# Kernel optimization log

Measured on AMD Instinct MI355X. Metric: run time of the kernel, lower is better.

The kernel has to match this reference:

```python
import jax, jax.numpy as jnp
import numpy as np

N, N_H = 256, 64          # detections per image, humans (permuted to top)
NUM_ITER = 2
E = 1024                   # node_encoding_size == box_feature_size
T_LIS, K_LIS, W_LIS = 8.3, 12.0, 10.0


def lis(x):
    # Low-grade Instance Suppression
    return T_LIS / (1.0 + jnp.exp(K_LIS - W_LIS * x))


def setup_inputs() -> dict:
    key = jax.random.key(0)
    ks = jax.random.split(key, 25)
    s = 0.02  # weight scale keeps sigmoid/relu in a sane range
    rn = lambda k, shape, sc=1.0: jax.random.normal(k, shape, jnp.float32) * sc
    inp = {}
    inp['box_features'] = rn(ks[0], (N, 12544))            # [N, 256*7*7]
    inp['node_spatial'] = rn(ks[1], (N, 1024))             # conv spatial-head output
    inp['scores'] = jax.random.uniform(ks[2], (N,), jnp.float32)
    labels = jax.random.randint(ks[3], (N,), 1, 80)
    inp['labels'] = labels.at[:N_H].set(0)                 # humans (idx 0) on top
    inp['class_mask'] = jax.random.bernoulli(ks[4], 0.2, (80, 117))
    inp['W_bh1'] = rn(ks[5], (12544, 1024), s); inp['b_bh1'] = jnp.zeros((1024,), jnp.float32)
    inp['W_bh2'] = rn(ks[6], (1024, 1024), s);  inp['b_bh2'] = jnp.zeros((1024,), jnp.float32)
    inp['W_sa']  = rn(ks[7], (1024, 1024), s)
    inp['W_a1']  = rn(ks[8], (4096, 2048), s); inp['b_a1'] = jnp.zeros((2048,), jnp.float32)
    inp['W_a2']  = rn(ks[9], (2048, 1024), s); inp['b_a2'] = jnp.zeros((1024,), jnp.float32)
    inp['W_a3']  = rn(ks[10], (1024, 1), s);   inp['b_a3'] = jnp.zeros((1,), jnp.float32)
    inp['W_hm']  = rn(ks[11], (1024, 1024), s); inp['b_hm'] = jnp.zeros((1024,), jnp.float32)
    inp['W_om']  = rn(ks[12], (1024, 1024), s); inp['b_om'] = jnp.zeros((1024,), jnp.float32)
    inp['W_hu']  = rn(ks[13], (2048, 1024), s)
    inp['W_ou']  = rn(ks[14], (2048, 1024), s)
    return inp


def _keep_indices():
    xv, yv = np.meshgrid(np.arange(N_H), np.arange(N), indexing='ij')
    m = (xv != yv).ravel()
    return jnp.asarray(xv.ravel()[m]), jnp.asarray(yv.ravel()[m])


def reference(box_features, node_spatial, scores, W_bh1, b_bh1, W_bh2, b_bh2,
              W_sa, W_a1, b_a1, W_a2, b_a2, W_a3, b_a3,
              W_hm, b_hm, W_om, b_om, W_hu, W_ou, labels, class_mask):
    # box_head: Flatten -> Linear -> ReLU -> Linear -> ReLU
    enc = jax.nn.relu(box_features @ W_bh1 + b_bh1)
    enc = jax.nn.relu(enc @ W_bh2 + b_bh2)                 # [N, E]
    h_enc = enc[:N_H]                                      # [N_H, E]
    h_sp = node_spatial[:N_H]                              # [N_H, 1024]
    # spatial_attention on pairwise spatial differences (fixed across iters)
    diff = node_spatial[None, :, :] - h_sp[:, None, :]     # [N_H, N, 1024]
    h_to_o = jnp.einsum('hnd,de->hne', diff, W_sa)         # Linear, no bias
    o_to_h = -h_to_o
    adj = jnp.ones((N_H, N), enc.dtype)
    for _ in range(NUM_ITER):
        # adjacency MLP + sigmoid over all n_h*n pairs
        hf = jnp.concatenate([h_enc, h_sp], axis=1)        # [N_H, 2048]
        of = jnp.concatenate([enc, node_spatial], axis=1)  # [N, 2048]
        pair_in = jnp.concatenate([
            jnp.broadcast_to(hf[:, None, :], (N_H, N, 2 * E)),
            jnp.broadcast_to(of[None, :, :], (N_H, N, 2 * E))], axis=-1)  # [N_H,N,4096]
        hdn = jax.nn.relu(pair_in @ W_a1 + b_a1)
        hdn = jax.nn.relu(hdn @ W_a2 + b_a2)
        adj = jax.nn.sigmoid((hdn @ W_a3 + b_a3)[..., 0])  # [N_H, N]
        # object -> human messages
        obj_msg = jax.nn.relu(enc @ W_om + b_om)           # [N, R]
        agg_o = (adj[..., None] * (obj_msg[None, :, :] * o_to_h)).sum(1)  # [N_H, R]
        h_enc = jnp.concatenate([h_enc, agg_o], axis=1) @ W_hu            # [N_H, E]
        # human -> object messages
        hum_msg = jax.nn.relu(h_enc @ W_hm + b_hm)         # [N_H, R]
        agg_h = (adj[..., None] * (hum_msg[:, None, :] * h_to_o)).sum(0)  # [N, R]
        enc = jnp.concatenate([enc, agg_h], axis=1) @ W_ou                # [N, E]
    x_keep, y_keep = _keep_indices()                       # [P], P = N_H*N - N_H
    pair_feats = jnp.concatenate([h_enc[x_keep], h_sp[x_keep],
                                  enc[y_keep], node_spatial[y_keep]], axis=1)  # [P, 4096]
    # prior scores: LIS(score_h)*LIS(score_o) scattered to valid target classes
    prod = lis(scores[x_keep]) * lis(scores[y_keep])       # [P]
    prior = prod[:, None] * class_mask[labels[y_keep]].astype(pair_feats.dtype)  # [P, 117]
    prior = adj[x_keep, y_keep][:, None] * prior
    return jnp.concatenate([pair_feats, prior], axis=1)    # [P, 4096+117]
```

## Files before the change

### kernel.cpp

```cpp
#include <hip/hip_runtime.h>

using bf16 = __bf16;
typedef __bf16 bf16x4 __attribute__((ext_vector_type(4)));
typedef __bf16 bf16x8 __attribute__((ext_vector_type(8)));
typedef float  f32x4  __attribute__((ext_vector_type(4)));

#define LDS_STRIDE 40
#define GST 40

__device__ __forceinline__ float ldf(const void* p, size_t i, int f32) {
    return f32 ? ((const float*)p)[i] : (float)((const bf16*)p)[i];
}
__device__ __forceinline__ bf16x8 ld8(const void* p, size_t i, int f32) {
    bf16x8 r;
    if (f32) {
        f32x4 a = *(const f32x4*)((const float*)p + i);
        f32x4 b = *(const f32x4*)((const float*)p + i + 4);
#pragma unroll
        for (int j = 0; j < 4; ++j) { r[j] = (bf16)a[j]; r[j + 4] = (bf16)b[j]; }
    } else {
        r = *(const bf16x8*)((const bf16*)p + i);
    }
    return r;
}
__device__ __forceinline__ void st1(void* p, size_t i, float v, int f32) {
    if (f32) ((float*)p)[i] = v;
    else     ((bf16*)p)[i] = (bf16)v;
}

__global__ void init_flag(int* __restrict__ dflag) { *dflag = 0; }

__global__ void detect_kernel(const unsigned short* __restrict__ p, int n,
                              int* __restrict__ dflag)
{
    const unsigned int* q = (const unsigned int*)p;
    const int nw = n >> 1;
    int hit = 0;
    for (int i = blockIdx.x * 256 + threadIdx.x; i < nw; i += gridDim.x * 256) {
        unsigned int w = q[i];
        if ((w & 0x7F80u) == 0x7F80u || (w & 0x7F800000u) == 0x7F800000u) hit = 1;
    }
    if (__any(hit) && (threadIdx.x & 63) == 0) atomicOr(dflag, 1);
}

__global__ void cvt_kernel(const void* __restrict__ src, bf16* __restrict__ dst,
                           int n, const int* __restrict__ dflag)
{
    const int f32 = *dflag;
    const int stride = gridDim.x * 256;
    if ((n & 7) == 0) {
        const int nv = n >> 3;
        for (int i = blockIdx.x * 256 + threadIdx.x; i < nv; i += stride) {
            bf16x8 v = ld8(src, (size_t)i * 8, f32);
            *(bf16x8*)(dst + (size_t)i * 8) = v;
        }
    } else {
        for (int i = blockIdx.x * 256 + threadIdx.x; i < n; i += stride)
            dst[i] = (bf16)ldf(src, i, f32);
    }
}

__global__ void transpose_any(const void* __restrict__ W, bf16* __restrict__ Wt,
                              int K, int N, const int* __restrict__ dflag)
{
    __shared__ bf16 tile[32][33];
    const int f32 = *dflag;
    const int n0 = blockIdx.x * 32, k0 = blockIdx.y * 32;
    const int tx = threadIdx.x, ty = threadIdx.y;
#pragma unroll
    for (int i = 0; i < 4; ++i)
        tile[ty + i * 8][tx] = (bf16)ldf(W, (size_t)(k0 + ty + i * 8) * N + n0 + tx, f32);
    __syncthreads();
#pragma unroll
    for (int i = 0; i < 4; ++i)
        Wt[(size_t)(n0 + ty + i * 8) * K + k0 + tx] = tile[tx][ty + i * 8];
}

__global__ __launch_bounds__(256)
void gemm_p(const bf16* __restrict__ A, int lda,
            const void* __restrict__ B, size_t boff, int ldb,
            float* __restrict__ part, int N, int Kc,
            const int* __restrict__ dflag)
{
    __shared__ bf16 As[64 * GST];
    __shared__ bf16 Bs[64 * GST];
    const int f32 = *dflag;
    const int t = threadIdx.x;
    const int l = t & 63;
    const int quad = l >> 4, lr = l & 15;
    const int w = t >> 6, wm = w >> 1, wn = w & 1;
    const int mBlock = blockIdx.y * 64, nBlock = blockIdx.x * 64;
    const int ar = t >> 2, ac = (t & 3) * 8;
    const int kr = t >> 3, nc = (t & 7) * 8;
    const int kBeg = blockIdx.z * Kc;
    const int nIter = Kc >> 5;

    f32x4 acc[2][2] = {};

    bf16x8 avr = *(const bf16x8*)(A + (size_t)(mBlock + ar) * lda + kBeg + ac);
    bf16x8 bvr = ld8(B, boff + (size_t)(kBeg + kr) * ldb + nBlock + nc, f32);

    for (int it = 0; it < nIter; ++it) {
        *(bf16x8*)&As[ar * GST + ac] = avr;
#pragma unroll
        for (int j = 0; j < 8; ++j) {
            int wr = nc + j;
            Bs[wr * GST + (kr ^ (((wr >> 3) & 3) << 3))] = bvr[j];
        }
        __syncthreads();
        if (it + 1 < nIter) {
            int k0 = kBeg + (it + 1) * 32;
            avr = *(const bf16x8*)(A + (size_t)(mBlock + ar) * lda + k0 + ac);
            bvr = ld8(B, boff + (size_t)(k0 + kr) * ldb + nBlock + nc, f32);
        }
        bf16x8 af[2], bfr[2];
#pragma unroll
        for (int mi = 0; mi < 2; ++mi)
            af[mi] = *(const bf16x8*)&As[(wm * 32 + mi * 16 + lr) * GST + quad * 8];
#pragma unroll
        for (int nj = 0; nj < 2; ++nj) {
            int row = wn * 32 + nj * 16 + lr;
            bfr[nj] = *(const bf16x8*)&Bs[row * GST + ((quad * 8) ^ (((row >> 3) & 3) << 3))];
        }
#pragma unroll
        for (int mi = 0; mi < 2; ++mi)
#pragma unroll
            for (int nj = 0; nj < 2; ++nj)
                acc[mi][nj] = __builtin_amdgcn_mfma_f32_16x16x32_bf16(
                    af[mi], bfr[nj], acc[mi][nj], 0, 0, 0);
        __syncthreads();
    }

    float* outp = part + (size_t)blockIdx.z * ((size_t)gridDim.y * 64 * N);
#pragma unroll
    for (int mi = 0; mi < 2; ++mi)
#pragma unroll
        for (int nj = 0; nj < 2; ++nj) {
            int col = nBlock + wn * 32 + nj * 16 + lr;
#pragma unroll
            for (int rr = 0; rr < 4; ++rr) {
                int row = mBlock + wm * 32 + mi * 16 + quad * 4 + rr;
                outp[(size_t)row * N + col] = acc[mi][nj][rr];
            }
        }
}

template<bool RELU, bool BIAS, bool F32OUT>
__global__ void reduce_k(const float* __restrict__ part, int S, int total,
                         const bf16* __restrict__ bias, void* __restrict__ out, int N)
{
    int base = (blockIdx.x * 256 + threadIdx.x) * 4;
    if (base >= total) return;
    f32x4 s = *(const f32x4*)(part + base);
    for (int z = 1; z < S; ++z) {
        f32x4 v = *(const f32x4*)(part + (size_t)z * total + base);
        s[0] += v[0]; s[1] += v[1]; s[2] += v[2]; s[3] += v[3];
    }
    int col = base % N;
#pragma unroll
    for (int j = 0; j < 4; ++j) {
        float v = s[j];
        if (BIAS) v += (float)bias[col + j];
        if (RELU) v = fmaxf(v, 0.f);
        if (F32OUT) ((float*)out)[base + j] = v;
        else        ((bf16*)out)[base + j] = (bf16)v;
    }
}

__global__ __launch_bounds__(256)
void pair_gemm(const float* __restrict__ Hpart, const float* __restrict__ Opart,
               const bf16* __restrict__ b_a1, const bf16* __restrict__ Wt_a2,
               const bf16* __restrict__ b_a2, const bf16* __restrict__ w_a3,
               float* __restrict__ slots)
{
    __shared__ bf16 As[128 * LDS_STRIDE];
    __shared__ bf16 Bs[128 * LDS_STRIDE];
    const int t = threadIdx.x;
    const int l = t & 63, w = t >> 6;
    const int quad = l >> 4, lr = l & 15;
    const int wm = w >> 1, wn = w & 1;
    const int nb = blockIdx.x, mb = blockIdx.y;
    const int p0 = mb * 128;
    const int h = p0 >> 8;
    const int nBase = p0 & 255;
    const int ar = t >> 1, ac0 = (t & 1) * 16;
    const float* Hrow = Hpart + h * 2048;
    const float* Orow = Opart + (size_t)(nBase + ar) * 2048;

    f32x4 acc[4][4] = {};

    for (int k0 = 0; k0 < 2048; k0 += 32) {
        __syncthreads();
        {
            const float* hp = Hrow + k0 + ac0;
            const float* op = Orow + k0 + ac0;
            f32x4 h0 = *(const f32x4*)(hp);
            f32x4 h1 = *(const f32x4*)(hp + 4);
            f32x4 h2 = *(const f32x4*)(hp + 8);
            f32x4 h3 = *(const f32x4*)(hp + 12);
            f32x4 o0 = *(const f32x4*)(op);
            f32x4 o1 = *(const f32x4*)(op + 4);
            f32x4 o2 = *(const f32x4*)(op + 8);
            f32x4 o3 = *(const f32x4*)(op + 12);
            bf16x8 r0, r1;
#pragma unroll
            for (int j = 0; j < 4; ++j) {
                r0[j]     = (bf16)fmaxf(h0[j] + o0[j] + (float)b_a1[k0 + ac0 + j],      0.f);
                r0[j + 4] = (bf16)fmaxf(h1[j] + o1[j] + (float)b_a1[k0 + ac0 + 4 + j],  0.f);
                r1[j]     = (bf16)fmaxf(h2[j] + o2[j] + (float)b_a1[k0 + ac0 + 8 + j],  0.f);
                r1[j + 4] = (bf16)fmaxf(h3[j] + o3[j] + (float)b_a1[k0 + ac0 + 12 + j], 0.f);
            }
            *(bf16x8*)&As[ar * LDS_STRIDE + ac0]     = r0;
            *(bf16x8*)&As[ar * LDS_STRIDE + ac0 + 8] = r1;
        }
#pragma unroll
        for (int i = 0; i < 2; ++i) {
            int idx = t + i * 256;
            int r = idx >> 2, c = (idx & 3) * 8;
            *(bf16x8*)&Bs[r * LDS_STRIDE + c] =
                *(const bf16x8*)(Wt_a2 + (size_t)(nb * 128 + r) * 2048 + k0 + c);
        }
        __syncthreads();

        bf16x8 af[4], bfr[4];
#pragma unroll
        for (int mi = 0; mi < 4; ++mi)
            af[mi] = *(const bf16x8*)&As[(wm * 64 + mi * 16 + lr) * LDS_STRIDE + quad * 8];
#pragma unroll
        for (int nj = 0; nj < 4; ++nj)
            bfr[nj] = *(const bf16x8*)&Bs[(wn * 64 + nj * 16 + lr) * LDS_STRIDE + quad * 8];
#pragma unroll
        for (int mi = 0; mi < 4; ++mi)
#pragma unroll
            for (int nj = 0; nj < 4; ++nj)
                acc[mi][nj] = __builtin_amdgcn_mfma_f32_16x16x32_bf16(
                    af[mi], bfr[nj], acc[mi][nj], 0, 0, 0);
    }

    float w3v[4], b2v[4];
#pragma unroll
    for (int nj = 0; nj < 4; ++nj) {
        int col = nb * 128 + wn * 64 + nj * 16 + lr;
        w3v[nj] = (float)w_a3[col];
        b2v[nj] = (float)b_a2[col];
    }
#pragma unroll
    for (int mi = 0; mi < 4; ++mi) {
        f32x4 rs = {0.f, 0.f, 0.f, 0.f};
#pragma unroll
        for (int nj = 0; nj < 4; ++nj)
#pragma unroll
            for (int rr = 0; rr < 4; ++rr)
                rs[rr] += fmaxf(acc[mi][nj][rr] + b2v[nj], 0.f) * w3v[nj];
#pragma unroll
        for (int off = 1; off < 16; off <<= 1) {
            rs[0] += __shfl_xor(rs[0], off);
            rs[1] += __shfl_xor(rs[1], off);
            rs[2] += __shfl_xor(rs[2], off);
            rs[3] += __shfl_xor(rs[3], off);
        }
        if (lr == 0) {
            int p = p0 + wm * 64 + mi * 16 + quad * 4;
            int slot = nb * 2 + wn;
            slots[(size_t)(p + 0) * 16 + slot] = rs[0];
            slots[(size_t)(p + 1) * 16 + slot] = rs[1];
            slots[(size_t)(p + 2) * 16 + slot] = rs[2];
            slots[(size_t)(p + 3) * 16 + slot] = rs[3];
        }
    }
}

__global__ void adj_finalize(const float* __restrict__ slots,
                             const bf16* __restrict__ b_a3, float* __restrict__ adj)
{
    int i = blockIdx.x * 256 + threadIdx.x;
    float s = (float)b_a3[0];
#pragma unroll
    for (int k = 0; k < 16; ++k) s += slots[(size_t)i * 16 + k];
    adj[i] = 1.f / (1.f + expf(-s));
}

__global__ void copy_rows(const bf16* __restrict__ src, int lds_,
                          bf16* __restrict__ dst, int ldd)
{
    int c = blockIdx.x * 256 + threadIdx.x;
    int r = blockIdx.y;
    dst[(size_t)r * ldd + c] = src[(size_t)r * lds_ + c];
}

__global__ void agg_o_kernel(const float* __restrict__ adj, const bf16* __restrict__ obj_msg,
                             const bf16* __restrict__ nsW, bf16* __restrict__ out)
{
    int e = blockIdx.x * 256 + threadIdx.x;
    int h = blockIdx.y;
    float nh = (float)nsW[h * 1024 + e];
    float s = 0.f;
    for (int n = 0; n < 256; ++n) {
        float a  = adj[h * 256 + n];
        float om = (float)obj_msg[n * 1024 + e];
        float nw = (float)nsW[n * 1024 + e];
        s += a * om * (nh - nw);
    }
    out[(size_t)h * 2048 + e] = (bf16)s;
}

__global__ void agg_h_kernel(const float* __restrict__ adj, const bf16* __restrict__ hum_msg,
                             const bf16* __restrict__ nsW, bf16* __restrict__ out)
{
    int e = blockIdx.x * 256 + threadIdx.x;
    int n = blockIdx.y;
    float nn = (float)nsW[n * 1024 + e];
    float s = 0.f;
    for (int h = 0; h < 64; ++h) {
        float a  = adj[h * 256 + n];
        float hm = (float)hum_msg[h * 1024 + e];
        float nw = (float)nsW[h * 1024 + e];
        s += a * hm * (nn - nw);
    }
    out[(size_t)n * 2048 + e] = (bf16)s;
}

__global__ void out_kernel(const bf16* __restrict__ h_enc, const bf16* __restrict__ enc,
                           const bf16* __restrict__ nsp_bf, const float* __restrict__ adj,
                           const bf16* __restrict__ scores_bf, const int* __restrict__ labels,
                           const int* __restrict__ cmask, void* __restrict__ out,
                           const int* __restrict__ dflag)
{
    const int f32 = *dflag;
    const int r = blockIdx.x;
    const int x = r / 255;
    const int tt = r % 255;
    const int y = tt + (tt >= x ? 1 : 0);
    const size_t rbase = (size_t)r * 4213;
    const bf16* seg[4] = { h_enc + x * 1024, nsp_bf + x * 1024, enc + y * 1024, nsp_bf + y * 1024 };
    const int t = threadIdx.x;
#pragma unroll
    for (int k = 0; k < 4; ++k) {
        int ci = t + k * 256;
        int sidx = ci >> 8;
        int off = (ci & 255) * 4;
        bf16x4 v = *(const bf16x4*)(seg[sidx] + off);
        size_t d = rbase + sidx * 1024 + off;
        st1(out, d + 0, (float)v[0], f32);
        st1(out, d + 1, (float)v[1], f32);
        st1(out, d + 2, (float)v[2], f32);
        st1(out, d + 3, (float)v[3], f32);
    }
    if (t < 117) {
        float sx = (float)scores_bf[x], sy = (float)scores_bf[y];
        float lx = 8.3f / (1.f + expf(12.f - 10.f * sx));
        float ly = 8.3f / (1.f + expf(12.f - 10.f * sy));
        float a = adj[x * 256 + y];
        float m = cmask[labels[y] * 117 + t] ? 1.f : 0.f;
        st1(out, rbase + 4096 + t, a * lx * ly * m, f32);
    }
}

extern "C" void kernel_launch(void* const* d_in, const int* in_sizes, int n_in,
                              void* d_out, int out_size, void* d_ws, size_t ws_size,
                              hipStream_t stream)
{
    (void)in_sizes; (void)n_in; (void)out_size; (void)ws_size;
    const void* box    = d_in[0];
    const void* nsp    = d_in[1];
    const void* scores = d_in[2];
    const int*  labels = (const int*)d_in[3];
    const int*  cmask  = (const int*)d_in[4];
    const void* W_bh1 = d_in[5],  *b_bh1 = d_in[6];
    const void* W_bh2 = d_in[7],  *b_bh2 = d_in[8];
    const void* W_sa  = d_in[9];
    const void* W_a1  = d_in[10], *b_a1  = d_in[11];
    const void* W_a2  = d_in[12], *b_a2  = d_in[13];
    const void* W_a3  = d_in[14], *b_a3  = d_in[15];
    const void* W_hm  = d_in[16], *b_hm  = d_in[17];
    const void* W_om  = d_in[18], *b_om  = d_in[19];
    const void* W_hu  = d_in[20];
    const void* W_ou  = d_in[21];

    char* ws = (char*)d_ws;
    size_t off = 0;
    auto alloc = [&](size_t bytes) -> void* {
        off = (off + 255) & ~(size_t)255;
        void* p = ws + off;
        off += bytes;
        return p;
    };
    int*  dflag   = (int*)alloc(4);
    bf16* box_bf  = (bf16*)alloc((size_t)256 * 12544 * 2);
    bf16* nsp_bf  = (bf16*)alloc((size_t)256 * 1024 * 2);
    bf16* Wt_a2   = (bf16*)alloc((size_t)1024 * 2048 * 2);
    bf16* smalls  = (bf16*)alloc((size_t)8464 * 2);
    bf16* sb_bh1 = smalls,        *sb_bh2 = smalls + 1024;
    bf16* sb_om  = smalls + 2048, *sb_hm  = smalls + 3072;
    bf16* sb_a1  = smalls + 4096, *sb_a2  = smalls + 6144;
    bf16* sw_a3  = smalls + 7168, *sb_a3  = smalls + 8192;
    bf16* sscore = smalls + 8208;
    bf16* t0      = (bf16*)alloc((size_t)256 * 1024 * 2);
    bf16* enc     = (bf16*)alloc((size_t)256 * 1024 * 2);
    bf16* nsW     = (bf16*)alloc((size_t)256 * 1024 * 2);
    bf16* h_enc   = (bf16*)alloc((size_t)64 * 1024 * 2);
    bf16* hf      = (bf16*)alloc((size_t)64 * 2048 * 2);
    bf16* of      = (bf16*)alloc((size_t)256 * 2048 * 2);
    float* Hpart  = (float*)alloc((size_t)64 * 2048 * 4);
    float* Opart  = (float*)alloc((size_t)256 * 2048 * 4);
    float* slots  = (float*)alloc((size_t)16384 * 16 * 4);
    float* adj    = (float*)alloc((size_t)16384 * 4);
    bf16* obj_msg = (bf16*)alloc((size_t)256 * 1024 * 2);
    bf16* hu_in   = (bf16*)alloc((size_t)64 * 2048 * 2);
    bf16* hum_msg = (bf16*)alloc((size_t)64 * 1024 * 2);
    bf16* ou_in   = (bf16*)alloc((size_t)256 * 2048 * 2);
    float* part   = (float*)alloc((size_t)2097152 * 4);

    init_flag<<<1, 1, 0, stream>>>(dflag);
    detect_kernel<<<256, 256, 0, stream>>>((const unsigned short*)box, 524288, dflag);

    auto cvt = [&](const void* s, bf16* d, int n) {
        int g = (n + 2047) / 2048; if (g < 1) g = 1; if (g > 4096) g = 4096;
        cvt_kernel<<<g, 256, 0, stream>>>(s, d, n, dflag);
    };
    cvt(box, box_bf, 256 * 12544);
    cvt(nsp, nsp_bf, 256 * 1024);
    cvt(b_bh1, sb_bh1, 1024);  cvt(b_bh2, sb_bh2, 1024);
    cvt(b_om,  sb_om,  1024);  cvt(b_hm,  sb_hm,  1024);
    cvt(b_a1,  sb_a1,  2048);  cvt(b_a2,  sb_a2,  1024);
    cvt(W_a3,  sw_a3,  1024);  cvt(b_a3,  sb_a3,  1);
    cvt(scores, sscore, 256);

    transpose_any<<<dim3(1024 / 32, 2048 / 32), dim3(32, 8), 0, stream>>>(
        W_a2, Wt_a2, 2048, 1024, dflag);

    gemm_p<<<dim3(16, 4, 8), 256, 0, stream>>>(box_bf, 12544, W_bh1, 0, 1024, part, 1024, 1568, dflag);
    reduce_k<true, true, false><<<dim3(256), 256, 0, stream>>>(part, 8, 262144, sb_bh1, t0, 1024);
    gemm_p<<<dim3(16, 4, 4), 256, 0, stream>>>(t0, 1024, W_bh2, 0, 1024, part, 1024, 256, dflag);
    reduce_k<true, true, false><<<dim3(256), 256, 0, stream>>>(part, 4, 262144, sb_bh2, enc, 1024);
    gemm_p<<<dim3(16, 4, 4), 256, 0, stream>>>(nsp_bf, 1024, W_sa, 0, 1024, part, 1024, 256, dflag);
    reduce_k<false, false, false><<<dim3(256), 256, 0, stream>>>(part, 4, 262144, nullptr, nsW, 1024);
    copy_rows<<<dim3(4, 64), 256, 0, stream>>>(enc, 1024, h_enc, 1024);

    for (int it = 0; it < 2; ++it) {
        copy_rows<<<dim3(4, 64), 256, 0, stream>>>(h_enc, 1024, hf, 2048);
        copy_rows<<<dim3(4, 64), 256, 0, stream>>>(nsp_bf, 1024, hf + 1024, 2048);
        copy_rows<<<dim3(4, 256), 256, 0, stream>>>(enc, 1024, of, 2048);
        copy_rows<<<dim3(4, 256), 256, 0, stream>>>(nsp_bf, 1024, of + 1024, 2048);
        gemm_p<<<dim3(32, 1, 8), 256, 0, stream>>>(hf, 2048, W_a1, 0, 2048, part, 2048, 256, dflag);
        reduce_k<false, false, true><<<dim3(128), 256, 0, stream>>>(part, 8, 131072, nullptr, Hpart, 2048);
        gemm_p<<<dim3(32, 4, 4), 256, 0, stream>>>(of, 2048, W_a1, (size_t)2048 * 2048, 2048, part, 2048, 512, dflag);
        reduce_k<false, false, true><<<dim3(512), 256, 0, stream>>>(part, 4, 524288, nullptr, Opart, 2048);
        pair_gemm<<<dim3(8, 128), 256, 0, stream>>>(Hpart, Opart, sb_a1, Wt_a2, sb_a2, sw_a3, slots);
        adj_finalize<<<dim3(64), 256, 0, stream>>>(slots, sb_a3, adj);
        gemm_p<<<dim3(16, 4, 4), 256, 0, stream>>>(enc, 1024, W_om, 0, 1024, part, 1024, 256, dflag);
        reduce_k<true, true, false><<<dim3(256), 256, 0, stream>>>(part, 4, 262144, sb_om, obj_msg, 1024);
        copy_rows<<<dim3(4, 64), 256, 0, stream>>>(h_enc, 1024, hu_in, 2048);
        agg_o_kernel<<<dim3(4, 64), 256, 0, stream>>>(adj, obj_msg, nsW, hu_in + 1024);
        gemm_p<<<dim3(16, 1, 16), 256, 0, stream>>>(hu_in, 2048, W_hu, 0, 1024, part, 1024, 128, dflag);
        reduce_k<false, false, false><<<dim3(64), 256, 0, stream>>>(part, 16, 65536, nullptr, h_enc, 1024);
        gemm_p<<<dim3(16, 1, 16), 256, 0, stream>>>(h_enc, 1024, W_hm, 0, 1024, part, 1024, 64, dflag);
        reduce_k<true, true, false><<<dim3(64), 256, 0, stream>>>(part, 16, 65536, sb_hm, hum_msg, 1024);
        copy_rows<<<dim3(4, 256), 256, 0, stream>>>(enc, 1024, ou_in, 2048);
        agg_h_kernel<<<dim3(4, 256), 256, 0, stream>>>(adj, hum_msg, nsW, ou_in + 1024);
        gemm_p<<<dim3(16, 4, 4), 256, 0, stream>>>(ou_in, 2048, W_ou, 0, 1024, part, 1024, 512, dflag);
        reduce_k<false, false, false><<<dim3(256), 256, 0, stream>>>(part, 4, 262144, nullptr, enc, 1024);
    }

    out_kernel<<<dim3(16320), 256, 0, stream>>>(
        h_enc, enc, nsp_bf, adj, sscore, labels, cmask, d_out, dflag);
}
```

Before: 1.152 ms.

## Materialize pair activations in bf16 and prefetch tiles in pair GEMM

```diff
diff --git a/kernel.cpp b/kernel.cpp
--- a/kernel.cpp
+++ b/kernel.cpp
@@ -167,9 +167,27 @@
     }
 }
 
+__global__ void build_pairA(const float* __restrict__ Hb, const float* __restrict__ Op,
+                            bf16* __restrict__ A)
+{
+    const int n = blockIdx.x;
+    const int h = blockIdx.y;
+    const int k = threadIdx.x * 8;
+    const float* hp = Hb + (size_t)h * 2048 + k;
+    const float* op = Op + (size_t)n * 2048 + k;
+    f32x4 h0 = *(const f32x4*)hp, h1 = *(const f32x4*)(hp + 4);
+    f32x4 o0 = *(const f32x4*)op, o1 = *(const f32x4*)(op + 4);
+    bf16x8 r;
+#pragma unroll
+    for (int j = 0; j < 4; ++j) {
+        r[j]     = (bf16)fmaxf(h0[j] + o0[j], 0.f);
+        r[j + 4] = (bf16)fmaxf(h1[j] + o1[j], 0.f);
+    }
+    *(bf16x8*)(A + ((size_t)h * 256 + n) * 2048 + k) = r;
+}
+
 __global__ __launch_bounds__(256)
-void pair_gemm(const float* __restrict__ Hpart, const float* __restrict__ Opart,
-               const bf16* __restrict__ b_a1, const bf16* __restrict__ Wt_a2,
+void pair_gemm(const bf16* __restrict__ Apg, const bf16* __restrict__ Wt_a2,
                const bf16* __restrict__ b_a2, const bf16* __restrict__ w_a3,
                float* __restrict__ slots)
 {
@@ -181,46 +199,30 @@
     const int wm = w >> 1, wn = w & 1;
     const int nb = blockIdx.x, mb = blockIdx.y;
     const int p0 = mb * 128;
-    const int h = p0 >> 8;
-    const int nBase = p0 & 255;
     const int ar = t >> 1, ac0 = (t & 1) * 16;
-    const float* Hrow = Hpart + h * 2048;
-    const float* Orow = Opart + (size_t)(nBase + ar) * 2048;
+
+    const bf16* Ap = Apg + (size_t)(p0 + ar) * 2048 + ac0;
+    const bf16* Bp = Wt_a2 + (size_t)(nb * 128 + ar) * 2048 + ac0;
 
     f32x4 acc[4][4] = {};
 
+    bf16x8 a0 = *(const bf16x8*)(Ap);
+    bf16x8 a1 = *(const bf16x8*)(Ap + 8);
+    bf16x8 b0 = *(const bf16x8*)(Bp);
+    bf16x8 b1 = *(const bf16x8*)(Bp + 8);
+
     for (int k0 = 0; k0 < 2048; k0 += 32) {
+        *(bf16x8*)&As[ar * LDS_STRIDE + ac0]     = a0;
+        *(bf16x8*)&As[ar * LDS_STRIDE + ac0 + 8] = a1;
+        *(bf16x8*)&Bs[ar * LDS_STRIDE + ac0]     = b0;
+        *(bf16x8*)&Bs[ar * LDS_STRIDE + ac0 + 8] = b1;
         __syncthreads();
-        {
-            const float* hp = Hrow + k0 + ac0;
-            const float* op = Orow + k0 + ac0;
-            f32x4 h0 = *(const f32x4*)(hp);
-            f32x4 h1 = *(const f32x4*)(hp + 4);
-            f32x4 h2 = *(const f32x4*)(hp + 8);
-            f32x4 h3 = *(const f32x4*)(hp + 12);
-            f32x4 o0 = *(const f32x4*)(op);
-            f32x4 o1 = *(const f32x4*)(op + 4);
-            f32x4 o2 = *(const f32x4*)(op + 8);
-            f32x4 o3 = *(const f32x4*)(op + 12);
-            bf16x8 r0, r1;
-#pragma unroll
-            for (int j = 0; j < 4; ++j) {
-                r0[j]     = (bf16)fmaxf(h0[j] + o0[j] + (float)b_a1[k0 + ac0 + j],      0.f);
-                r0[j + 4] = (bf16)fmaxf(h1[j] + o1[j] + (float)b_a1[k0 + ac0 + 4 + j],  0.f);
-                r1[j]     = (bf16)fmaxf(h2[j] + o2[j] + (float)b_a1[k0 + ac0 + 8 + j],  0.f);
-                r1[j + 4] = (bf16)fmaxf(h3[j] + o3[j] + (float)b_a1[k0 + ac0 + 12 + j], 0.f);
-            }
-            *(bf16x8*)&As[ar * LDS_STRIDE + ac0]     = r0;
-            *(bf16x8*)&As[ar * LDS_STRIDE + ac0 + 8] = r1;
-        }
-#pragma unroll
-        for (int i = 0; i < 2; ++i) {
-            int idx = t + i * 256;
-            int r = idx >> 2, c = (idx & 3) * 8;
-            *(bf16x8*)&Bs[r * LDS_STRIDE + c] =
-                *(const bf16x8*)(Wt_a2 + (size_t)(nb * 128 + r) * 2048 + k0 + c);
-        }
-        __syncthreads();
+        if (k0 + 32 < 2048) {
+            a0 = *(const bf16x8*)(Ap + k0 + 32);
+            a1 = *(const bf16x8*)(Ap + k0 + 40);
+            b0 = *(const bf16x8*)(Bp + k0 + 32);
+            b1 = *(const bf16x8*)(Bp + k0 + 40);
+        }
 
         bf16x8 af[4], bfr[4];
 #pragma unroll
@@ -235,6 +237,7 @@
             for (int nj = 0; nj < 4; ++nj)
                 acc[mi][nj] = __builtin_amdgcn_mfma_f32_16x16x32_bf16(
                     af[mi], bfr[nj], acc[mi][nj], 0, 0, 0);
+        __syncthreads();
     }
 
     float w3v[4], b2v[4];
@@ -410,6 +413,7 @@
     bf16* hum_msg = (bf16*)alloc((size_t)64 * 1024 * 2);
     bf16* ou_in   = (bf16*)alloc((size_t)256 * 2048 * 2);
     float* part   = (float*)alloc((size_t)2097152 * 4);
+    bf16* A_bf    = (bf16*)alloc((size_t)16384 * 2048 * 2);
 
     init_flag<<<1, 1, 0, stream>>>(dflag);
     detect_kernel<<<256, 256, 0, stream>>>((const unsigned short*)box, 524288, dflag);
@@ -443,10 +447,11 @@
         copy_rows<<<dim3(4, 256), 256, 0, stream>>>(enc, 1024, of, 2048);
         copy_rows<<<dim3(4, 256), 256, 0, stream>>>(nsp_bf, 1024, of + 1024, 2048);
         gemm_p<<<dim3(32, 1, 8), 256, 0, stream>>>(hf, 2048, W_a1, 0, 2048, part, 2048, 256, dflag);
-        reduce_k<false, false, true><<<dim3(128), 256, 0, stream>>>(part, 8, 131072, nullptr, Hpart, 2048);
+        reduce_k<false, true, true><<<dim3(128), 256, 0, stream>>>(part, 8, 131072, sb_a1, Hpart, 2048);
         gemm_p<<<dim3(32, 4, 4), 256, 0, stream>>>(of, 2048, W_a1, (size_t)2048 * 2048, 2048, part, 2048, 512, dflag);
         reduce_k<false, false, true><<<dim3(512), 256, 0, stream>>>(part, 4, 524288, nullptr, Opart, 2048);
-        pair_gemm<<<dim3(8, 128), 256, 0, stream>>>(Hpart, Opart, sb_a1, Wt_a2, sb_a2, sw_a3, slots);
+        build_pairA<<<dim3(256, 64), 256, 0, stream>>>(Hpart, Opart, A_bf);
+        pair_gemm<<<dim3(8, 128), 256, 0, stream>>>(A_bf, Wt_a2, sb_a2, sw_a3, slots);
         adj_finalize<<<dim3(64), 256, 0, stream>>>(slots, sb_a3, adj);
         gemm_p<<<dim3(16, 4, 4), 256, 0, stream>>>(enc, 1024, W_om, 0, 1024, part, 1024, 256, dflag);
         reduce_k<true, true, false><<<dim3(256), 256, 0, stream>>>(part, 4, 262144, sb_om, obj_msg, 1024);
```

Result: faster. 1.031 ms (-10.5%).
